# Kernel tuning notes

Hardware: AMD Instinct MI355X
Metric: run time of the kernel (lower is better)

The kernel has to match this reference:

```python
import jax, jax.numpy as jnp
import numpy as np

NUM_GRAPHS = 100
NODES_PER_GRAPH = 400
UND_EDGES_PER_GRAPH = 5000  # -> 10000 directed edges per graph
UNITS = 64


def setup_inputs() -> dict:
    rng = np.random.default_rng(0)
    g = np.repeat(np.arange(NUM_GRAPHS), UND_EDGES_PER_GRAPH)
    src_l = rng.integers(0, NODES_PER_GRAPH, g.shape[0])
    dst_l = rng.integers(0, NODES_PER_GRAPH, g.shape[0])
    # avoid self loops (molecular graphs have none by default)
    dst_l = np.where(dst_l == src_l, (dst_l + 1) % NODES_PER_GRAPH, dst_l)
    src = (g * NODES_PER_GRAPH + src_l).astype(np.int32)
    dst = (g * NODES_PER_GRAPH + dst_l).astype(np.int32)
    # both directions, as produced by molecular graph encoders
    edge_src = jnp.asarray(np.concatenate([src, dst]))
    edge_dst = jnp.asarray(np.concatenate([dst, src]))
    E = edge_src.shape[0]
    num_nodes = NUM_GRAPHS * NODES_PER_GRAPH
    graph_indicator = jnp.asarray(
        np.repeat(np.arange(NUM_GRAPHS), NODES_PER_GRAPH).astype(np.int32))
    key = jax.random.key(0)
    k1, k2 = jax.random.split(key)
    edge_feature = jax.random.normal(k1, (E, UNITS), dtype=jnp.float32)
    W = jax.random.normal(k2, (2 * UNITS, UNITS), dtype=jnp.float32) * 0.005
    b = jnp.zeros((UNITS,), dtype=jnp.float32)
    return {"edge_feature": edge_feature, "edge_src": edge_src,
            "edge_dst": edge_dst, "graph_indicator": graph_indicator,
            "num_nodes": num_nodes, "W": W, "b": b}


def _reverse_edge_features(edge_feature, edge_src, edge_dst, num_nodes):
    # For each edge i, sum of edge_feature[j] over all j with
    # (src_j, dst_j) == (dst_i, src_i). Node ids are disjoint across
    # subgraphs, so a global (src,dst) key match is equivalent to the
    # per-subgraph match done by the original tf.map_fn version.
    E = edge_feature.shape[0]
    key = edge_src * num_nodes + edge_dst          # fits int32 for N<=46k
    rev = edge_dst * num_nodes + edge_src
    perm = jnp.argsort(key)
    sk = key[perm]
    # group duplicate keys (multi-edges) and sum their features
    new_grp = jnp.concatenate(
        [jnp.zeros((1,), sk.dtype), (sk[1:] != sk[:-1]).astype(sk.dtype)])
    gid = jnp.cumsum(new_grp)                      # [E] group id per sorted edge
    group_sum = jax.ops.segment_sum(edge_feature[perm], gid, num_segments=E)
    pos = jnp.clip(jnp.searchsorted(sk, rev), 0, E - 1)
    match = sk[pos] == rev
    return jnp.where(match[:, None], group_sum[gid[pos]], 0.0)


def reference(edge_feature, edge_src, edge_dst, graph_indicator, num_nodes, W, b):
    # message step: aggregate incoming edge states at each node, gather back
    # to each edge's source node, subtract the reverse edge's own state
    agg = jax.ops.segment_sum(edge_feature, edge_dst, num_segments=num_nodes)
    message = agg[edge_src] - _reverse_edge_features(
        edge_feature, edge_src, edge_dst, num_nodes)
    # update step: Dense(relu) on concat([prev_state, message])
    h = jnp.concatenate([edge_feature, message], axis=1)
    return jax.nn.relu(h @ W + b)
```

## Files before the change

kernel.cpp:

```cpp
#include <hip/hip_runtime.h>
#include <cstdint>
#include <cstddef>

#define OA_LOG 21
static constexpr unsigned OA_SLOTS = 1u << OA_LOG;
static constexpr unsigned OA_MASK  = OA_SLOTS - 1;
static constexpr unsigned HASH_MUL = 2654435761u;
static constexpr unsigned GSZ = 400;
static constexpr unsigned DENSE_DUP = 0xFFFFFFFFu;

typedef __attribute__((ext_vector_type(8))) short short8;
typedef __attribute__((ext_vector_type(4))) float floatx4;

union U4S8 { uint4 u; short8 s; };

__device__ inline unsigned bf16rn(float x) {
    unsigned u = __float_as_uint(x);
    return (u + 0x7FFFu + ((u >> 16) & 1u)) >> 16;
}
__device__ inline unsigned pk2(float a, float b) {
    return bf16rn(a) | (bf16rn(b) << 16);
}

__global__ void wpack_kernel(const float* __restrict__ W, uint4* __restrict__ wsW) {
    const int lane = threadIdx.x;
    const int n = lane & 15, q = lane >> 4;
    for (int s = 0; s < 4; ++s)
        for (int t = 0; t < 4; ++t) {
            unsigned dw[4];
#pragma unroll
            for (int jj = 0; jj < 4; ++jj) {
                float a = W[(32 * s + 8 * q + 2 * jj) * 64 + 16 * t + n];
                float b = W[(32 * s + 8 * q + 2 * jj + 1) * 64 + 16 * t + n];
                dw[jj] = pk2(a, b);
            }
            wsW[(s * 4 + t) * 64 + lane] = make_uint4(dw[0], dw[1], dw[2], dw[3]);
        }
}

__global__ void prep_build_kernel(const int* __restrict__ esrc,
                                  const int* __restrict__ edst,
                                  int* __restrict__ cnt,
                                  unsigned long long* __restrict__ tbl,
                                  unsigned* __restrict__ dense,
                                  int E, unsigned NN) {
    int e = blockIdx.x * blockDim.x + threadIdx.x;
    if (e >= E) return;
    const unsigned s = (unsigned)esrc[e], d = (unsigned)edst[e];
    atomicAdd(&cnt[d], 1);

    unsigned k = s * NN + d;
    unsigned long long mine = ((unsigned long long)(unsigned)e << 32) | (unsigned long long)k;
    unsigned slot = (k * HASH_MUL) >> (32 - OA_LOG);
    const unsigned long long EMPTY = ~0ull;
    while (atomicCAS(&tbl[slot], EMPTY, mine) != EMPTY)
        slot = (slot + 1) & OA_MASK;

    if (dense) {
        const unsigned gs = s / GSZ, gd = d / GSZ;
        if (gs == gd) {
            unsigned dk = s * GSZ + (d - gd * GSZ);
            unsigned old = atomicCAS(&dense[dk], 0u, (unsigned)e + 1u);
            if (old != 0u) atomicExch(&dense[dk], DENSE_DUP);
        }
    }
}

__global__ void scan_kernel(int* __restrict__ cnt, int* __restrict__ off, int NN, int E) {
    __shared__ int sd[1024];
    const int t = threadIdx.x;
    const int chunk = (NN + 1023) >> 10;
    const int lo = t * chunk, hi = min(lo + chunk, NN);
    int local = 0;
    for (int i = lo; i < hi; ++i) local += cnt[i];
    sd[t] = local;
    __syncthreads();
    for (int s = 1; s < 1024; s <<= 1) {
        int v = (t >= s) ? sd[t - s] : 0;
        __syncthreads();
        sd[t] += v;
        __syncthreads();
    }
    int run = sd[t] - local;
    for (int i = lo; i < hi; ++i) {
        int c = cnt[i];
        off[i] = run;
        cnt[i] = run;
        run += c;
    }
    if (t == 0) off[NN] = E;
}

__global__ void scatter_kernel(const int* __restrict__ edst, int* __restrict__ cursor,
                               int* __restrict__ csr, int E) {
    int e = blockIdx.x * blockDim.x + threadIdx.x;
    if (e >= E) return;
    int slot = atomicAdd(&cursor[edst[e]], 1);
    csr[slot] = e;
}

__global__ void mark_rev_kernel(const int* __restrict__ esrc,
                                const int* __restrict__ edst,
                                const unsigned long long* __restrict__ tbl,
                                int* __restrict__ revid,
                                int E, unsigned NN) {
    int e = blockIdx.x * blockDim.x + threadIdx.x;
    if (e >= E) return;
    unsigned rk = (unsigned)edst[e] * NN + (unsigned)esrc[e];
    unsigned s = (rk * HASH_MUL) >> (32 - OA_LOG);
    int cnt = 0, idx = -1;
    while (true) {
        unsigned long long v = tbl[s];
        if ((unsigned)v == 0xFFFFFFFFu) break;
        if ((unsigned)v == rk) { ++cnt; idx = (int)(v >> 32); }
        s = (s + 1) & OA_MASK;
    }
    revid[e] = (cnt == 1) ? idx : -1;
}

__global__ __launch_bounds__(256)
void agg_csr_kernel(const float* __restrict__ feat, const int* __restrict__ csr,
                    const int* __restrict__ off, float* __restrict__ agg, int NN) {
    const int wid = (blockIdx.x * blockDim.x + threadIdx.x) >> 6;
    const int lane = threadIdx.x & 63;
    if (wid >= NN) return;
    const int i0 = off[wid], i1 = off[wid + 1];
    float acc = 0.f;
    int i = i0;
    for (; i + 8 <= i1; i += 8) {
        int c[8];
#pragma unroll
        for (int j = 0; j < 8; ++j) c[j] = csr[i + j];
        float a[8];
#pragma unroll
        for (int j = 0; j < 8; ++j) a[j] = feat[((long long)c[j] << 6) + lane];
        acc += ((a[0] + a[1]) + (a[2] + a[3])) + ((a[4] + a[5]) + (a[6] + a[7]));
    }
    for (; i < i1; ++i) acc += feat[((long long)csr[i] << 6) + lane];
    agg[((long long)wid << 6) + lane] = acc;
}

__global__ __launch_bounds__(256, 4)
void fused_kernel(const float* __restrict__ feat,
                  const int* __restrict__ esrc,
                  const int* __restrict__ edst,
                  const float* __restrict__ agg,
                  const unsigned long long* __restrict__ tbl,
                  const unsigned* __restrict__ dense,
                  const int* __restrict__ revid,
                  int use_dense,
                  const uint4* __restrict__ wsW,
                  const float* __restrict__ bias,
                  float* __restrict__ out,
                  int E, unsigned NN) {
    __shared__ unsigned lds_h[64 * 68];
    const int tid = threadIdx.x;
    const int lane = tid & 63;
    const int n = lane & 15;
    const int q = lane >> 4;
    const int g = blockIdx.x;
    const long long H = (long long)(E >> 1);
    const bool paired = (E & 63) == 0;

    const int el = tid >> 2;
    const int p = tid & 3;
    long long e;
    if (paired) e = (long long)g * 32 + (el & 31) + (long long)(el >> 5) * H;
    else        e = (long long)g * 64 + el;

    float4 f0, f1, f2, f3, m0, m1, m2, m3;
    if (e < (long long)E) {
        const float4* fp = (const float4*)(feat + (e << 6) + 16 * p);
        f0 = fp[0]; f1 = fp[1]; f2 = fp[2]; f3 = fp[3];
        const int s_ = esrc[e], d_ = edst[e];
        const float4* ap = (const float4*)(agg + ((long long)s_ << 6) + 16 * p);
        m0 = ap[0]; m1 = ap[1]; m2 = ap[2]; m3 = ap[3];

        int rid = -1;
        bool slow = false;
        if (use_dense) {
            const unsigned gs = (unsigned)s_ / GSZ, gd = (unsigned)d_ / GSZ;
            if (gs == gd) {
                unsigned v = dense[(unsigned)d_ * GSZ + ((unsigned)s_ - gs * GSZ)];
                if (v == 0u) {  }
                else if (v == DENSE_DUP) slow = true;
                else rid = (int)(v - 1u);
            } else slow = true;
        } else {
            rid = revid[e];
            if (rid < 0) slow = true;
        }

        float4 r0, r1, r2, r3;
        r0 = r1 = r2 = r3 = make_float4(0.f, 0.f, 0.f, 0.f);
        if (rid >= 0) {
            const float4* rp = (const float4*)(feat + ((long long)rid << 6) + 16 * p);
            r0 = rp[0]; r1 = rp[1]; r2 = rp[2]; r3 = rp[3];
        } else if (slow) {
            const unsigned rk = (unsigned)d_ * NN + (unsigned)s_;
            unsigned slot = (rk * HASH_MUL) >> (32 - OA_LOG);
            while (true) {
                unsigned long long v = tbl[slot];
                if ((unsigned)v == 0xFFFFFFFFu) break;
                if ((unsigned)v == rk) {
                    const float4* rp =
                        (const float4*)(feat + ((long long)(v >> 32) << 6) + 16 * p);
                    float4 a0 = rp[0], a1 = rp[1], a2 = rp[2], a3 = rp[3];
                    r0.x += a0.x; r0.y += a0.y; r0.z += a0.z; r0.w += a0.w;
                    r1.x += a1.x; r1.y += a1.y; r1.z += a1.z; r1.w += a1.w;
                    r2.x += a2.x; r2.y += a2.y; r2.z += a2.z; r2.w += a2.w;
                    r3.x += a3.x; r3.y += a3.y; r3.z += a3.z; r3.w += a3.w;
                }
                slot = (slot + 1) & OA_MASK;
            }
        }
        m0.x -= r0.x; m0.y -= r0.y; m0.z -= r0.z; m0.w -= r0.w;
        m1.x -= r1.x; m1.y -= r1.y; m1.z -= r1.z; m1.w -= r1.w;
        m2.x -= r2.x; m2.y -= r2.y; m2.z -= r2.z; m2.w -= r2.w;
        m3.x -= r3.x; m3.y -= r3.y; m3.z -= r3.z; m3.w -= r3.w;
    } else {
        f0 = f1 = f2 = f3 = make_float4(0.f, 0.f, 0.f, 0.f);
        m0 = m1 = m2 = m3 = make_float4(0.f, 0.f, 0.f, 0.f);
    }
    unsigned* row = &lds_h[el * 68];
    *(uint4*)(row + 8 * p) =
        make_uint4(pk2(f0.x, f0.y), pk2(f0.z, f0.w), pk2(f1.x, f1.y), pk2(f1.z, f1.w));
    *(uint4*)(row + 8 * p + 4) =
        make_uint4(pk2(f2.x, f2.y), pk2(f2.z, f2.w), pk2(f3.x, f3.y), pk2(f3.z, f3.w));
    *(uint4*)(row + 32 + 8 * p) =
        make_uint4(pk2(m0.x, m0.y), pk2(m0.z, m0.w), pk2(m1.x, m1.y), pk2(m1.z, m1.w));
    *(uint4*)(row + 32 + 8 * p + 4) =
        make_uint4(pk2(m2.x, m2.y), pk2(m2.z, m2.w), pk2(m3.x, m3.y), pk2(m3.z, m3.w));
    __syncthreads();

    short8 wf[4][4];
#pragma unroll
    for (int s = 0; s < 4; ++s)
#pragma unroll
        for (int t = 0; t < 4; ++t) {
            U4S8 cvt;
            cvt.u = wsW[(s * 4 + t) * 64 + lane];
            wf[s][t] = cvt.s;
        }
    float bv[4];
#pragma unroll
    for (int t = 0; t < 4; ++t) bv[t] = bias[16 * t + n];

    const int w = tid >> 6;
    floatx4 acc[4];
#pragma unroll
    for (int t = 0; t < 4; ++t) acc[t] = (floatx4){0.f, 0.f, 0.f, 0.f};
#pragma unroll
    for (int s = 0; s < 4; ++s) {
        U4S8 a;
        a.u = *(const uint4*)&lds_h[(16 * w + n) * 68 + 16 * s + 4 * q];
#pragma unroll
        for (int t = 0; t < 4; ++t)
            acc[t] = __builtin_amdgcn_mfma_f32_16x16x32_bf16(a.s, wf[s][t], acc[t], 0, 0, 0);
    }

#pragma unroll
    for (int r = 0; r < 4; ++r) {
        const int rowi = 16 * w + 4 * q + r;
        long long ee;
        if (paired) ee = (long long)g * 32 + (rowi & 31) + (long long)(rowi >> 5) * H;
        else        ee = (long long)g * 64 + rowi;
        if (ee < (long long)E) {
#pragma unroll
            for (int t = 0; t < 4; ++t) {
                float v = acc[t][r] + bv[t];
                out[(ee << 6) + 16 * t + n] = v > 0.f ? v : 0.f;
            }
        }
    }
}

extern "C" void kernel_launch(void* const* d_in, const int* in_sizes, int n_in,
                              void* d_out, int out_size, void* d_ws, size_t ws_size,
                              hipStream_t stream) {
    const float* feat = (const float*)d_in[0];
    const int*   esrc = (const int*)d_in[1];
    const int*   edst = (const int*)d_in[2];
    const float* W    = (const float*)d_in[5];
    const float* bias = (const float*)d_in[6];
    float* out = (float*)d_out;

    const int E  = in_sizes[1];
    const int NN = in_sizes[3];

    char* ws = (char*)d_ws;
    size_t o = 0;
    auto alloc = [&](size_t bytes) { void* p = ws + o; o = (o + bytes + 15) & ~(size_t)15; return p; };
    float* agg   = (float*)alloc((size_t)NN * 64 * sizeof(float));
    int*   cnt   = (int*)alloc((size_t)NN * sizeof(int));
    int*   off   = (int*)alloc((size_t)(NN + 1) * sizeof(int));
    int*   csr   = (int*)alloc((size_t)E * sizeof(int));
    unsigned long long* tbl = (unsigned long long*)alloc((size_t)OA_SLOTS * 8);
    uint4* wsW   = (uint4*)alloc((size_t)16 * 64 * sizeof(uint4));
    int*   revid = (int*)alloc((size_t)E * sizeof(int));
    const size_t dense_elems = (size_t)NN * GSZ;
    unsigned* dense = (unsigned*)alloc(dense_elems * sizeof(unsigned));
    const int use_dense = (o <= ws_size) ? 1 : 0;

    hipMemsetAsync(cnt, 0, (size_t)NN * sizeof(int), stream);
    hipMemsetAsync(tbl, 0xFF, (size_t)OA_SLOTS * 8, stream);
    if (use_dense)
        hipMemsetAsync(dense, 0, dense_elems * sizeof(unsigned), stream);

    const int eb = (E + 255) / 256;
    wpack_kernel<<<1, 64, 0, stream>>>(W, wsW);
    prep_build_kernel<<<eb, 256, 0, stream>>>(esrc, edst, cnt, tbl,
                                              use_dense ? dense : nullptr, E, (unsigned)NN);
    scan_kernel<<<1, 1024, 0, stream>>>(cnt, off, NN, E);
    scatter_kernel<<<eb, 256, 0, stream>>>(edst, cnt, csr, E);
    if (!use_dense)
        mark_rev_kernel<<<eb, 256, 0, stream>>>(esrc, edst, tbl, revid, E, (unsigned)NN);
    agg_csr_kernel<<<(NN + 3) / 4, 256, 0, stream>>>(feat, csr, off, agg, NN);
    fused_kernel<<<(E + 63) / 64, 256, 0, stream>>>(
        feat, esrc, edst, agg, tbl, dense, revid, use_dense, wsW, bias, out, E, (unsigned)NN);
}
```

Baseline: 905.2 us.

## Replace dense reverse-edge table with bitmaps and verified mirror-index fast path

Drops the NN×400 32-bit dense reverse-edge table and its large memset. Two small bitmaps (seen, duplicate) are built instead, plus a per-edge byte code that marks each edge as having no reverse, a verified mirror reverse at e±E/2, or needing a hash probe. Hash-table insertion now happens only for edges that some probe may need, and scatter and reverse classification are merged into one pass. The aim is to cut memset bandwidth, scattered 32-bit atomics and hash-insert contention. The cost is a second pass over the edges, and correctness now depends on the mirror and insertion logic staying consistent.

```diff
diff --git a/kernel.cpp b/kernel.cpp
--- a/kernel.cpp
+++ b/kernel.cpp
@@ -7,7 +7,9 @@
 static constexpr unsigned OA_MASK  = OA_SLOTS - 1;
 static constexpr unsigned HASH_MUL = 2654435761u;
 static constexpr unsigned GSZ = 400;
-static constexpr unsigned DENSE_DUP = 0xFFFFFFFFu;
+static constexpr unsigned char RC_ZERO   = 0;
+static constexpr unsigned char RC_MIRROR = 1;
+static constexpr unsigned char RC_PROBE  = 2;
 
 typedef __attribute__((ext_vector_type(8))) short short8;
 typedef __attribute__((ext_vector_type(4))) float floatx4;
@@ -38,31 +40,22 @@
         }
 }
 
-__global__ void prep_build_kernel(const int* __restrict__ esrc,
-                                  const int* __restrict__ edst,
-                                  int* __restrict__ cnt,
-                                  unsigned long long* __restrict__ tbl,
-                                  unsigned* __restrict__ dense,
-                                  int E, unsigned NN) {
+__global__ void prep1_kernel(const int* __restrict__ esrc,
+                             const int* __restrict__ edst,
+                             int* __restrict__ cnt,
+                             unsigned* __restrict__ seen,
+                             unsigned* __restrict__ dupb,
+                             int E) {
     int e = blockIdx.x * blockDim.x + threadIdx.x;
     if (e >= E) return;
     const unsigned s = (unsigned)esrc[e], d = (unsigned)edst[e];
     atomicAdd(&cnt[d], 1);
-
-    unsigned k = s * NN + d;
-    unsigned long long mine = ((unsigned long long)(unsigned)e << 32) | (unsigned long long)k;
-    unsigned slot = (k * HASH_MUL) >> (32 - OA_LOG);
-    const unsigned long long EMPTY = ~0ull;
-    while (atomicCAS(&tbl[slot], EMPTY, mine) != EMPTY)
-        slot = (slot + 1) & OA_MASK;
-
-    if (dense) {
-        const unsigned gs = s / GSZ, gd = d / GSZ;
-        if (gs == gd) {
-            unsigned dk = s * GSZ + (d - gd * GSZ);
-            unsigned old = atomicCAS(&dense[dk], 0u, (unsigned)e + 1u);
-            if (old != 0u) atomicExch(&dense[dk], DENSE_DUP);
-        }
+    const unsigned gs = s / GSZ, gd = d / GSZ;
+    if (gs == gd) {
+        unsigned dk = s * GSZ + (d - gd * GSZ);
+        unsigned w = dk >> 5, b = 1u << (dk & 31);
+        unsigned old = atomicOr(&seen[w], b);
+        if (old & b) atomicOr(&dupb[w], b);
     }
 }
 
@@ -91,31 +84,52 @@
     if (t == 0) off[NN] = E;
 }
 
-__global__ void scatter_kernel(const int* __restrict__ edst, int* __restrict__ cursor,
-                               int* __restrict__ csr, int E) {
+__global__ void prep2_kernel(const int* __restrict__ esrc,
+                             const int* __restrict__ edst,
+                             int* __restrict__ cursor,
+                             int* __restrict__ csr,
+                             const unsigned* __restrict__ seen,
+                             const unsigned* __restrict__ dupb,
+                             unsigned long long* __restrict__ tbl,
+                             unsigned char* __restrict__ rcode,
+                             int E, unsigned NN) {
     int e = blockIdx.x * blockDim.x + threadIdx.x;
     if (e >= E) return;
-    int slot = atomicAdd(&cursor[edst[e]], 1);
+    const unsigned s = (unsigned)esrc[e], d = (unsigned)edst[e];
+    int slot = atomicAdd(&cursor[d], 1);
     csr[slot] = e;
-}
-
-__global__ void mark_rev_kernel(const int* __restrict__ esrc,
-                                const int* __restrict__ edst,
-                                const unsigned long long* __restrict__ tbl,
-                                int* __restrict__ revid,
-                                int E, unsigned NN) {
-    int e = blockIdx.x * blockDim.x + threadIdx.x;
-    if (e >= E) return;
-    unsigned rk = (unsigned)edst[e] * NN + (unsigned)esrc[e];
-    unsigned s = (rk * HASH_MUL) >> (32 - OA_LOG);
-    int cnt = 0, idx = -1;
-    while (true) {
-        unsigned long long v = tbl[s];
-        if ((unsigned)v == 0xFFFFFFFFu) break;
-        if ((unsigned)v == rk) { ++cnt; idx = (int)(v >> 32); }
-        s = (s + 1) & OA_MASK;
-    }
-    revid[e] = (cnt == 1) ? idx : -1;
+
+    const bool even = (E & 1) == 0;
+    const int H = E >> 1;
+    bool ins;
+    unsigned char code;
+    const unsigned gs = s / GSZ, gd = d / GSZ;
+    if (even && gs == gd) {
+        const int m = (e < H) ? e + H : e - H;
+        const unsigned sm = (unsigned)esrc[m], dm = (unsigned)edst[m];
+        const bool mok = (sm == d) && (dm == s);
+        const unsigned dk = s * GSZ + (d - gd * GSZ);
+        const unsigned rk = d * GSZ + (s - gs * GSZ);
+        const bool dupK  = (dupb[dk >> 5] >> (dk & 31)) & 1u;
+        const bool seenR = (seen[rk >> 5] >> (rk & 31)) & 1u;
+        const bool dupR  = (dupb[rk >> 5] >> (rk & 31)) & 1u;
+        ins  = dupK || dupR || !mok;
+        code = !seenR ? RC_ZERO : (dupR ? RC_PROBE : (mok ? RC_MIRROR : RC_PROBE));
+    } else {
+        ins = true;
+        code = RC_PROBE;
+    }
+    rcode[e] = code;
+
+    if (ins) {
+        const unsigned k = s * NN + d;
+        unsigned long long mine =
+            ((unsigned long long)(unsigned)e << 32) | (unsigned long long)k;
+        unsigned sl = (k * HASH_MUL) >> (32 - OA_LOG);
+        const unsigned long long EMPTY = ~0ull;
+        while (atomicCAS(&tbl[sl], EMPTY, mine) != EMPTY)
+            sl = (sl + 1) & OA_MASK;
+    }
 }
 
 __global__ __launch_bounds__(256)
@@ -146,9 +160,7 @@
                   const int* __restrict__ edst,
                   const float* __restrict__ agg,
                   const unsigned long long* __restrict__ tbl,
-                  const unsigned* __restrict__ dense,
-                  const int* __restrict__ revid,
-                  int use_dense,
+                  const unsigned char* __restrict__ rcode,
                   const uint4* __restrict__ wsW,
                   const float* __restrict__ bias,
                   float* __restrict__ out,
@@ -176,27 +188,14 @@
         const float4* ap = (const float4*)(agg + ((long long)s_ << 6) + 16 * p);
         m0 = ap[0]; m1 = ap[1]; m2 = ap[2]; m3 = ap[3];
 
-        int rid = -1;
-        bool slow = false;
-        if (use_dense) {
-            const unsigned gs = (unsigned)s_ / GSZ, gd = (unsigned)d_ / GSZ;
-            if (gs == gd) {
-                unsigned v = dense[(unsigned)d_ * GSZ + ((unsigned)s_ - gs * GSZ)];
-                if (v == 0u) {  }
-                else if (v == DENSE_DUP) slow = true;
-                else rid = (int)(v - 1u);
-            } else slow = true;
-        } else {
-            rid = revid[e];
-            if (rid < 0) slow = true;
-        }
-
+        const unsigned char code = rcode[e];
         float4 r0, r1, r2, r3;
         r0 = r1 = r2 = r3 = make_float4(0.f, 0.f, 0.f, 0.f);
-        if (rid >= 0) {
-            const float4* rp = (const float4*)(feat + ((long long)rid << 6) + 16 * p);
+        if (code == RC_MIRROR) {
+            const long long m = (e < H) ? e + H : e - H;
+            const float4* rp = (const float4*)(feat + (m << 6) + 16 * p);
             r0 = rp[0]; r1 = rp[1]; r2 = rp[2]; r3 = rp[3];
-        } else if (slow) {
+        } else if (code == RC_PROBE) {
             const unsigned rk = (unsigned)d_ * NN + (unsigned)s_;
             unsigned slot = (rk * HASH_MUL) >> (32 - OA_LOG);
             while (true) {
@@ -297,25 +296,22 @@
     int*   csr   = (int*)alloc((size_t)E * sizeof(int));
     unsigned long long* tbl = (unsigned long long*)alloc((size_t)OA_SLOTS * 8);
     uint4* wsW   = (uint4*)alloc((size_t)16 * 64 * sizeof(uint4));
-    int*   revid = (int*)alloc((size_t)E * sizeof(int));
-    const size_t dense_elems = (size_t)NN * GSZ;
-    unsigned* dense = (unsigned*)alloc(dense_elems * sizeof(unsigned));
-    const int use_dense = (o <= ws_size) ? 1 : 0;
+    const size_t bm_words = ((size_t)NN * GSZ + 31) / 32;
+    unsigned* seen = (unsigned*)alloc(bm_words * sizeof(unsigned));
+    unsigned* dupb = (unsigned*)alloc(bm_words * sizeof(unsigned));
+    unsigned char* rcode = (unsigned char*)alloc((size_t)E);
 
     hipMemsetAsync(cnt, 0, (size_t)NN * sizeof(int), stream);
     hipMemsetAsync(tbl, 0xFF, (size_t)OA_SLOTS * 8, stream);
-    if (use_dense)
-        hipMemsetAsync(dense, 0, dense_elems * sizeof(unsigned), stream);
+    hipMemsetAsync(seen, 0, 2 * bm_words * sizeof(unsigned), stream);
 
     const int eb = (E + 255) / 256;
     wpack_kernel<<<1, 64, 0, stream>>>(W, wsW);
-    prep_build_kernel<<<eb, 256, 0, stream>>>(esrc, edst, cnt, tbl,
-                                              use_dense ? dense : nullptr, E, (unsigned)NN);
+    prep1_kernel<<<eb, 256, 0, stream>>>(esrc, edst, cnt, seen, dupb, E);
     scan_kernel<<<1, 1024, 0, stream>>>(cnt, off, NN, E);
-    scatter_kernel<<<eb, 256, 0, stream>>>(edst, cnt, csr, E);
-    if (!use_dense)
-        mark_rev_kernel<<<eb, 256, 0, stream>>>(esrc, edst, tbl, revid, E, (unsigned)NN);
+    prep2_kernel<<<eb, 256, 0, stream>>>(esrc, edst, cnt, csr, seen, dupb, tbl,
+                                         rcode, E, (unsigned)NN);
     agg_csr_kernel<<<(NN + 3) / 4, 256, 0, stream>>>(feat, csr, off, agg, NN);
     fused_kernel<<<(E + 63) / 64, 256, 0, stream>>>(
-        feat, esrc, edst, agg, tbl, dense, revid, use_dense, wsW, bias, out, E, (unsigned)NN);
-}
+        feat, esrc, edst, agg, tbl, rcode, wsW, bias, out, E, (unsigned)NN);
+}
```

Result: faster. 769.1 us (-15.0%).
